# Kernel tuning notes

Measured on AMD Instinct MI355X. Metric: run time of the kernel, lower is better.

## Reference

```python
import jax, jax.numpy as jnp
import numpy as np

N, K, C, CL = 1024, 32, 64, 128
H = 2 * C  # MLP hidden = 2 * pair channels


def _ln(x, g, b, eps=1e-5):
    m = x.mean(-1, keepdims=True)
    v = jnp.mean(jnp.square(x - m), -1, keepdims=True)
    return (x - m) * jax.lax.rsqrt(v + eps) * g + b


def setup_inputs() -> dict:
    key = jax.random.key(0)
    ks = jax.random.split(key, 16)

    def w(k, shape):
        return jax.random.normal(k, shape, jnp.float32) / np.float32(np.sqrt(shape[0]))

    local = jax.random.normal(ks[0], (N, CL), jnp.float32)
    pair = jax.random.normal(ks[1], (N, N, C), jnp.float32)
    pair_update = jax.random.normal(ks[2], (N, K, C), jnp.float32)
    r = jax.random.randint(ks[3], (N, K), -(N // 4), N)
    neighbours = jnp.where(r < 0, -1, r)
    mask = jax.random.bernoulli(ks[4], 0.9, (N,))
    return dict(
        local=local, pair=pair, pair_update=pair_update,
        neighbours=neighbours, mask=mask,
        Wa=w(ks[5], (CL, C)), Wb=w(ks[6], (CL, C)),
        ln_g=jnp.ones((C,), jnp.float32), ln_b=jnp.zeros((C,), jnp.float32),
        W_aug=w(ks[7], (C, C)), W_lin=w(ks[8], (C, C)),
        W_left=w(ks[9], (C, 32)), b_left=jnp.zeros((32,), jnp.float32),
        W_right=w(ks[10], (C, 32)), b_right=jnp.zeros((32,), jnp.float32),
        W1=w(ks[11], (32, H)), W2=w(ks[12], (H, C)),
        W_int=w(ks[13], (CL, C)), b_int=jnp.zeros((C,), jnp.float32),
    )


def reference(local, pair, pair_update, neighbours, mask,
              Wa, Wb, ln_g, ln_b, W_aug, W_lin,
              W_left, b_left, W_right, b_right, W1, W2, W_int, b_int):
    idx = jnp.arange(pair.shape[0])
    # inject local info into the sparse pair update   [N,K,C]
    pu = pair_update + (local @ Wa)[:, None] + (local @ Wb)[neighbours]
    # gather neighbour pair features + layernorm      [N,K,C]
    lp = _ln(pair[idx[:, None], neighbours], ln_g, ln_b)
    lp = lp + pu @ W_aug
    linear = lp @ W_lin                               # [N,K,C]
    left = lp @ W_left + b_left                       # [N,K,32]
    right = lp @ W_right + b_right                    # [N,K,32]
    # neighbour-of-neighbour pair features            [N,K,K,32]
    npair = left[:, None] + right[neighbours]
    pn = neighbours[neighbours]                       # [N,K,K]
    pn = jnp.where((neighbours == -1)[:, :, None], pn, -1)
    pm = (pn != -1) & mask[pn] & (neighbours != -1)[:, None, :]
    # fused per-edge-pair MLP                          [N,K,K,C]
    upd = jax.nn.gelu(npair @ W1) @ W2
    # masked mean over the middle neighbour axis       [N,K,C]
    upd = jnp.where(pm[..., None], upd, 0.0).sum(axis=1)
    upd = upd / jnp.maximum(pm.sum(axis=1), 1).astype(upd.dtype)[..., None]
    inter = local @ W_int + b_int                     # [N,C]
    # scatter-add back into the dense pair tensor (collisions possible)
    return pair.at[idx[:, None], neighbours].add(upd + inter[:, None] + linear)
```

## Files before the change

### kernel.cpp

```cpp
#include <hip/hip_runtime.h>
#include <hip/hip_bf16.h>

constexpr int Nn  = 1024;
constexpr int Kk  = 32;
constexpr int Cc  = 64;
constexpr int CLl = 128;

__device__ __forceinline__ float gelu_tanh(float v){
  float c = 0.7978845608028654f*(v + 0.044715f*v*v*v);
  return 0.5f*v*(1.f + tanhf(c));
}

__global__ __launch_bounds__(64) void k0(
    const float* __restrict__ local, const float* __restrict__ Wa,
    const float* __restrict__ Wb, const float* __restrict__ Wint,
    const float* __restrict__ b_int,
    float* __restrict__ A, float* __restrict__ B, float* __restrict__ inter){
  int i = blockIdx.x;
  int c = threadIdx.x;
  __shared__ float l[CLl];
  l[c]      = local[i*CLl + c];
  l[c + 64] = local[i*CLl + 64 + c];
  __syncthreads();
  float a = 0.f, b = 0.f, t = 0.f;
  #pragma unroll 4
  for(int d = 0; d < CLl; ++d){
    float ld = l[d];
    a = fmaf(ld, Wa[d*Cc + c], a);
    b = fmaf(ld, Wb[d*Cc + c], b);
    t = fmaf(ld, Wint[d*Cc + c], t);
  }
  A[i*Cc + c] = a;
  B[i*Cc + c] = b;
  inter[i*Cc + c] = t + b_int[c];
}

__global__ __launch_bounds__(256) void k1(
    const float* __restrict__ pair, const float* __restrict__ pair_update,
    const int* __restrict__ neigh, const int* __restrict__ mask,
    const float* __restrict__ ln_g, const float* __restrict__ ln_b,
    const float* __restrict__ W_aug, const float* __restrict__ W_right,
    const float* __restrict__ b_right,
    const float* __restrict__ A, const float* __restrict__ B,
    float* __restrict__ r1023, int* __restrict__ qpart){
  const int i = Nn - 1;
  __shared__ float wA[4096];
  __shared__ float wR[2048];
  __shared__ float p [Kk][68];
  __shared__ float pu[Kk][68];
  __shared__ float lp[Kk][68];
  __shared__ int   nwS[Kk];
  __shared__ float ssum[Kk][9], ssq[Kk][9], stats[Kk][2];
  int tid = threadIdx.x;
  for(int idx = tid; idx < 4096; idx += 256) wA[idx] = W_aug[idx];
  for(int idx = tid; idx < 2048; idx += 256) wR[idx] = W_right[idx];
  if(tid < Kk){
    int n = neigh[i*Kk + tid];
    nwS[tid] = (n < 0) ? n + Nn : n;
    qpart[tid] = (n != -1 && mask[n] != 0) ? 1 : 0;
  }
  __syncthreads();
  int k = tid >> 3, s = tid & 7;
  {
    const float* prow = pair + ((size_t)i*Nn + nwS[k])*Cc + s*8;
    const float* pur  = pair_update + ((size_t)i*Kk + k)*Cc + s*8;
    const float* Ar = A + i*Cc + s*8;
    const float* Br = B + (size_t)nwS[k]*Cc + s*8;
    float ps = 0.f, ps2 = 0.f;
    for(int j = 0; j < 8; ++j){
      float v = prow[j];
      p[k][s*8 + j] = v; ps += v; ps2 += v*v;
      pu[k][s*8 + j] = pur[j] + Ar[j] + Br[j];
    }
    ssum[k][s] = ps; ssq[k][s] = ps2;
  }
  __syncthreads();
  if(s == 0){
    float m = 0.f, q = 0.f;
    for(int j = 0; j < 8; ++j){ m += ssum[k][j]; q += ssq[k][j]; }
    m *= (1.f/64.f); q *= (1.f/64.f);
    float var = fmaxf(q - m*m, 0.f);
    stats[k][0] = m; stats[k][1] = rsqrtf(var + 1e-5f);
  }
  __syncthreads();
  {
    float m = stats[k][0], r = stats[k][1];
    float acc[8];
    #pragma unroll
    for(int j = 0; j < 8; ++j){
      int c = s*8 + j;
      acc[j] = (p[k][c] - m)*r*ln_g[c] + ln_b[c];
    }
    for(int d = 0; d < 64; ++d){
      float pd = pu[k][d];
      #pragma unroll
      for(int j = 0; j < 8; ++j) acc[j] = fmaf(pd, wA[d*64 + s*8 + j], acc[j]);
    }
    #pragma unroll
    for(int j = 0; j < 8; ++j) lp[k][s*8 + j] = acc[j];
  }
  __syncthreads();
  {
    float acc[4] = {0.f,0.f,0.f,0.f};
    for(int d = 0; d < 64; ++d){
      float ld = lp[k][d];
      #pragma unroll
      for(int j = 0; j < 4; ++j) acc[j] = fmaf(ld, wR[d*32 + s*4 + j], acc[j]);
    }
    #pragma unroll
    for(int j = 0; j < 4; ++j)
      r1023[k*32 + s*4 + j] = acc[j] + b_right[s*4 + j];
  }
}

__global__ __launch_bounds__(256) void kcopy(
    const uint4* __restrict__ src, uint4* __restrict__ dst, int nvec){
  int idx = blockIdx.x*blockDim.x + threadIdx.x;
  int stride = gridDim.x*blockDim.x;
  for(; idx < nvec; idx += stride) dst[idx] = src[idx];
}

__global__ __launch_bounds__(256) void k2a(
    const float* __restrict__ pair, const float* __restrict__ pair_update,
    const int* __restrict__ neigh,
    const float* __restrict__ ln_g, const float* __restrict__ ln_b,
    const float* __restrict__ W_aug, const float* __restrict__ W_lin,
    const float* __restrict__ W_left, const float* __restrict__ b_left,
    const float* __restrict__ A, const float* __restrict__ B,
    const float* __restrict__ inter, const float* __restrict__ r1023,
    float* __restrict__ hG, float* __restrict__ linG){
  __shared__ float wA[4096];
  __shared__ float wL[4096];
  __shared__ float wF[2048];
  __shared__ float pbuf [Kk][68];
  __shared__ float pubuf[Kk][68];
  __shared__ float AiS[64], InS[64];
  __shared__ float ssum[Kk][9], ssq[Kk][9], stats[Kk][2];
  __shared__ int nwS[Kk];

  int i   = blockIdx.x;
  int tid = threadIdx.x;
  int k   = tid >> 3, s = tid & 7;

  for(int idx = tid; idx < 4096; idx += 256) wA[idx] = W_aug[idx];
  for(int idx = tid; idx < 4096; idx += 256) wL[idx] = W_lin[idx];
  for(int idx = tid; idx < 2048; idx += 256) wF[idx] = W_left[idx];
  if(tid < Kk){
    int n = neigh[i*Kk + tid];
    nwS[tid] = (n < 0) ? n + Nn : n;
  }
  if(tid < 64){ AiS[tid] = A[i*Cc + tid]; InS[tid] = inter[i*Cc + tid]; }
  __syncthreads();

  {
    const float4* p4 = (const float4*)(pair + ((size_t)i*Nn + nwS[k])*Cc) + s*2;
    float4 p0 = p4[0], p1 = p4[1];
    const float4* u4 = (const float4*)(pair_update + ((size_t)i*Kk + k)*Cc) + s*2;
    float4 u0 = u4[0], u1 = u4[1];
    const float4* Br = (const float4*)(B + (size_t)nwS[k]*Cc) + s*2;
    float4 b0 = Br[0], b1 = Br[1];
    float pf[8] = {p0.x,p0.y,p0.z,p0.w,p1.x,p1.y,p1.z,p1.w};
    float uf[8] = {u0.x,u0.y,u0.z,u0.w,u1.x,u1.y,u1.z,u1.w};
    float bv[8] = {b0.x,b0.y,b0.z,b0.w,b1.x,b1.y,b1.z,b1.w};
    float ps = 0.f, ps2 = 0.f;
    #pragma unroll
    for(int j = 0; j < 8; ++j){
      float v = pf[j];
      pbuf[k][s*8 + j] = v; ps += v; ps2 += v*v;
      pubuf[k][s*8 + j] = uf[j] + AiS[s*8 + j] + bv[j];
    }
    ssum[k][s] = ps; ssq[k][s] = ps2;
  }
  __syncthreads();

  if(s == 0){
    float m = 0.f, q = 0.f;
    for(int j = 0; j < 8; ++j){ m += ssum[k][j]; q += ssq[k][j]; }
    m *= (1.f/64.f); q *= (1.f/64.f);
    float var = fmaxf(q - m*m, 0.f);
    stats[k][0] = m; stats[k][1] = rsqrtf(var + 1e-5f);
  }
  __syncthreads();

  {
    float m = stats[k][0], r = stats[k][1];
    float acc[8];
    #pragma unroll
    for(int j = 0; j < 8; ++j){
      int c = s*8 + j;
      acc[j] = (pbuf[k][c] - m)*r*ln_g[c] + ln_b[c];
    }
    #pragma unroll 4
    for(int d = 0; d < 64; ++d){
      float pd = pubuf[k][d];
      #pragma unroll
      for(int j = 0; j < 8; ++j) acc[j] = fmaf(pd, wA[d*64 + s*8 + j], acc[j]);
    }
    #pragma unroll
    for(int j = 0; j < 8; ++j) pbuf[k][s*8 + j] = acc[j];
  }
  __syncthreads();

  {
    float accL[8] = {0,0,0,0,0,0,0,0};
    float accX[4] = {0,0,0,0};
    #pragma unroll 4
    for(int d = 0; d < 64; ++d){
      float ld = pbuf[k][d];
      #pragma unroll
      for(int j = 0; j < 8; ++j) accL[j] = fmaf(ld, wL[d*64 + s*8 + j], accL[j]);
      #pragma unroll
      for(int j = 0; j < 4; ++j) accX[j] = fmaf(ld, wF[d*32 + s*4 + j], accX[j]);
    }
    float4 rv = *(const float4*)(r1023 + k*32 + s*4);
    float rr[4] = {rv.x, rv.y, rv.z, rv.w};
    float* lo = linG + ((size_t)i*Kk + k)*Cc + s*8;
    #pragma unroll
    for(int j = 0; j < 8; ++j) lo[j] = accL[j] + InS[s*8 + j];
    float* ho = hG + ((size_t)i*Kk + k)*32 + s*4;
    #pragma unroll
    for(int j = 0; j < 4; ++j) ho[j] = accX[j] + b_left[s*4 + j] + rr[j];
  }
}

__global__ __launch_bounds__(256) void k2b(
    const float* __restrict__ pair, const int* __restrict__ neigh,
    const float* __restrict__ W1, const float* __restrict__ W2,
    const float* __restrict__ hG, const float* __restrict__ linG,
    const int* __restrict__ qpart,
    float* __restrict__ out){
  __shared__ float w1s[4096];
  __shared__ float w2s[8192];
  __shared__ float hbuf[Kk][36];
  __shared__ float cbuf[Kk][68];
  __shared__ int nbS[Kk], nwS[Kk], quS[Kk], leadS[Kk];
  __shared__ int cminus;

  int i   = blockIdx.x;
  int tid = threadIdx.x;
  int k   = tid >> 3, s = tid & 7;

  for(int idx = tid; idx < 4096; idx += 256) w1s[idx] = W1[idx];
  for(int idx = tid; idx < 8192; idx += 256) w2s[idx] = W2[idx];
  for(int idx = tid; idx < 1024; idx += 256)
    hbuf[idx >> 5][idx & 31] = hG[(size_t)i*1024 + idx];
  if(tid < Kk){
    int n = neigh[i*Kk + tid];
    nbS[tid] = n;
    nwS[tid] = (n < 0) ? n + Nn : n;
    quS[tid] = qpart[tid];
  }
  __syncthreads();
  if(tid == 0){
    int c = 0;
    for(int kk = 0; kk < Kk; ++kk) c |= (nbS[kk] == -1);
    cminus = c;
  }

  float gg[16];
  {
    float acc[16];
    #pragma unroll
    for(int j = 0; j < 16; ++j) acc[j] = 0.f;
    #pragma unroll 2
    for(int x = 0; x < 32; ++x){
      float hx = hbuf[k][x];
      #pragma unroll
      for(int j = 0; j < 16; ++j) acc[j] = fmaf(hx, w1s[x*128 + s*16 + j], acc[j]);
    }
    #pragma unroll
    for(int j = 0; j < 16; ++j) gg[j] = gelu_tanh(acc[j]);
  }
  __syncthreads();

  {
    float V[8] = {0,0,0,0,0,0,0,0};
    int klane = (k & 7) << 3;
    for(int ss = 0; ss < 8; ++ss){
      #pragma unroll
      for(int hh = 0; hh < 16; ++hh){
        float gv = __shfl(gg[hh], klane + ss, 64);
        int h = ss*16 + hh;
        #pragma unroll
        for(int j = 0; j < 8; ++j) V[j] = fmaf(gv, w2s[h*64 + s*8 + j], V[j]);
      }
    }
    const float4* l4 = (const float4*)(linG + ((size_t)i*Kk + k)*Cc) + s*2;
    float4 l0 = l4[0], l1 = l4[1];
    float lv[8] = {l0.x,l0.y,l0.z,l0.w,l1.x,l1.y,l1.z,l1.w};
    float mul = (cminus && quS[k] && nbS[k] != -1) ? 1.f : 0.f;
    #pragma unroll
    for(int j = 0; j < 8; ++j) cbuf[k][s*8 + j] = fmaf(mul, V[j], lv[j]);
  }
  __syncthreads();

  if(tid < Kk){
    int lead = 1;
    for(int kk = 0; kk < tid; ++kk) if(nwS[kk] == nwS[tid]) lead = 0;
    leadS[tid] = lead;
  }
  __syncthreads();
  if(leadS[k]){
    int col = nwS[k];
    float tot[8] = {0,0,0,0,0,0,0,0};
    for(int kk = 0; kk < Kk; ++kk){
      if(nwS[kk] == col){
        #pragma unroll
        for(int j = 0; j < 8; ++j) tot[j] += cbuf[kk][s*8 + j];
      }
    }
    size_t base = ((size_t)i*Nn + col)*Cc + s*8;
    const float4* pv = (const float4*)(pair + base);
    float4 p0 = pv[0], p1 = pv[1];
    float4 o0 = make_float4(p0.x+tot[0], p0.y+tot[1], p0.z+tot[2], p0.w+tot[3]);
    float4 o1 = make_float4(p1.x+tot[4], p1.y+tot[5], p1.z+tot[6], p1.w+tot[7]);
    float4* ov = (float4*)(out + base);
    ov[0] = o0; ov[1] = o1;
  }
}

extern "C" void kernel_launch(void* const* d_in, const int* in_sizes, int n_in,
                              void* d_out, int out_size, void* d_ws, size_t ws_size,
                              hipStream_t stream){
  (void)in_sizes; (void)n_in; (void)out_size; (void)ws_size;
  const float* local       = (const float*)d_in[0];
  const float* pair        = (const float*)d_in[1];
  const float* pair_update = (const float*)d_in[2];
  const int*   neighbours  = (const int*)d_in[3];
  const int*   mask        = (const int*)d_in[4];
  const float* Wa          = (const float*)d_in[5];
  const float* Wb          = (const float*)d_in[6];
  const float* ln_g        = (const float*)d_in[7];
  const float* ln_b        = (const float*)d_in[8];
  const float* W_aug       = (const float*)d_in[9];
  const float* W_lin       = (const float*)d_in[10];
  const float* W_left      = (const float*)d_in[11];
  const float* b_left      = (const float*)d_in[12];
  const float* W_right     = (const float*)d_in[13];
  const float* b_right     = (const float*)d_in[14];
  const float* W1          = (const float*)d_in[15];
  const float* W2          = (const float*)d_in[16];
  const float* W_int       = (const float*)d_in[17];
  const float* b_int       = (const float*)d_in[18];

  float* ws    = (float*)d_ws;
  float* A     = ws;
  float* B     = ws + 65536;
  float* inter = ws + 131072;
  float* r1023 = ws + 196608;
  int*   qpart = (int*)(ws + 197632);
  float* hG    = ws + 197664;
  float* linG  = ws + 1246240;

  k0<<<dim3(Nn), dim3(64), 0, stream>>>(local, Wa, Wb, W_int, b_int, A, B, inter);
  k1<<<dim3(1), dim3(256), 0, stream>>>(pair, pair_update, neighbours, mask,
                                        ln_g, ln_b, W_aug, W_right, b_right,
                                        A, B, r1023, qpart);
  k2a<<<dim3(Nn), dim3(256), 0, stream>>>(pair, pair_update, neighbours,
                                          ln_g, ln_b, W_aug, W_lin, W_left, b_left,
                                          A, B, inter, r1023, hG, linG);
  kcopy<<<dim3(8192), dim3(256), 0, stream>>>((const uint4*)pair, (uint4*)d_out,
                                              (Nn*Nn*Cc*4)/16);
  k2b<<<dim3(Nn), dim3(256), 0, stream>>>(pair, neighbours, W1, W2, hG, linG,
                                          qpart, (float*)d_out);
}
```

Baseline: 571.9 us.

## Fuse pair copy into update kernel and store weights as bf16 in LDS

Removes the separate full-tensor copy kernel: each block of the final kernel now copies its own row of the pair tensor to the output before scattering its updates, with a block barrier ordering the two writes. Weight matrices are converted to packed bf16 in shared memory, halving LDS footprint and load traffic. Threads are remapped so each one computes two neighbour rows, reusing every weight load across both. The bf16 weights lower accuracy of all the small matmuls, and the per-block copy is serialised with compute inside each block rather than run as a separate grid.

```diff
diff --git a/kernel.cpp b/kernel.cpp
--- a/kernel.cpp
+++ b/kernel.cpp
@@ -6,9 +6,20 @@
 constexpr int Cc  = 64;
 constexpr int CLl = 128;
 
+typedef unsigned int   u32;
+typedef unsigned short u16;
+
 __device__ __forceinline__ float gelu_tanh(float v){
   float c = 0.7978845608028654f*(v + 0.044715f*v*v*v);
   return 0.5f*v*(1.f + tanhf(c));
+}
+__device__ __forceinline__ float bflo(u32 u){ return __uint_as_float(u<<16); }
+__device__ __forceinline__ float bfhi(u32 u){ return __uint_as_float(u & 0xffff0000u); }
+__device__ __forceinline__ u32 pack_bf(float a, float b){
+  u32 xa = __float_as_uint(a), xb = __float_as_uint(b);
+  u32 ra = (xa + 0x7fffu + ((xa>>16)&1u)) >> 16;
+  u32 rb = (xb + 0x7fffu + ((xb>>16)&1u)) >> 16;
+  return ra | (rb<<16);
 }
 
 __global__ __launch_bounds__(64) void k0(
@@ -113,13 +124,6 @@
   }
 }
 
-__global__ __launch_bounds__(256) void kcopy(
-    const uint4* __restrict__ src, uint4* __restrict__ dst, int nvec){
-  int idx = blockIdx.x*blockDim.x + threadIdx.x;
-  int stride = gridDim.x*blockDim.x;
-  for(; idx < nvec; idx += stride) dst[idx] = src[idx];
-}
-
 __global__ __launch_bounds__(256) void k2a(
     const float* __restrict__ pair, const float* __restrict__ pair_update,
     const int* __restrict__ neigh,
@@ -129,35 +133,47 @@
     const float* __restrict__ A, const float* __restrict__ B,
     const float* __restrict__ inter, const float* __restrict__ r1023,
     float* __restrict__ hG, float* __restrict__ linG){
-  __shared__ float wA[4096];
-  __shared__ float wL[4096];
-  __shared__ float wF[2048];
+  __shared__ u32 wbA[2048];
+  __shared__ u32 wbL[2048];
+  __shared__ u32 wbF[1024];
   __shared__ float pbuf [Kk][68];
   __shared__ float pubuf[Kk][68];
-  __shared__ float AiS[64], InS[64];
+  __shared__ float AiS[64], InS[64], lgS[64], lbS[64];
   __shared__ float ssum[Kk][9], ssq[Kk][9], stats[Kk][2];
   __shared__ int nwS[Kk];
 
   int i   = blockIdx.x;
   int tid = threadIdx.x;
-  int k   = tid >> 3, s = tid & 7;
-
-  for(int idx = tid; idx < 4096; idx += 256) wA[idx] = W_aug[idx];
-  for(int idx = tid; idx < 4096; idx += 256) wL[idx] = W_lin[idx];
-  for(int idx = tid; idx < 2048; idx += 256) wF[idx] = W_left[idx];
+
+  for(int idx = tid; idx < 2048; idx += 256){
+    const float2 wa = *(const float2*)(W_aug + idx*2);
+    wbA[idx] = pack_bf(wa.x, wa.y);
+    const float2 wl = *(const float2*)(W_lin + idx*2);
+    wbL[idx] = pack_bf(wl.x, wl.y);
+  }
+  for(int idx = tid; idx < 1024; idx += 256){
+    const float2 wf = *(const float2*)(W_left + idx*2);
+    wbF[idx] = pack_bf(wf.x, wf.y);
+  }
   if(tid < Kk){
     int n = neigh[i*Kk + tid];
     nwS[tid] = (n < 0) ? n + Nn : n;
   }
-  if(tid < 64){ AiS[tid] = A[i*Cc + tid]; InS[tid] = inter[i*Cc + tid]; }
-  __syncthreads();
-
-  {
-    const float4* p4 = (const float4*)(pair + ((size_t)i*Nn + nwS[k])*Cc) + s*2;
+  if(tid < 64){
+    AiS[tid] = A[i*Cc + tid];
+    InS[tid] = inter[i*Cc + tid];
+    lgS[tid] = ln_g[tid];
+    lbS[tid] = ln_b[tid];
+  }
+  __syncthreads();
+
+  {
+    int k8 = tid >> 3, s8 = tid & 7;
+    const float4* p4 = (const float4*)(pair + ((size_t)i*Nn + nwS[k8])*Cc) + s8*2;
     float4 p0 = p4[0], p1 = p4[1];
-    const float4* u4 = (const float4*)(pair_update + ((size_t)i*Kk + k)*Cc) + s*2;
+    const float4* u4 = (const float4*)(pair_update + ((size_t)i*Kk + k8)*Cc) + s8*2;
     float4 u0 = u4[0], u1 = u4[1];
-    const float4* Br = (const float4*)(B + (size_t)nwS[k]*Cc) + s*2;
+    const float4* Br = (const float4*)(B + (size_t)nwS[k8]*Cc) + s8*2;
     float4 b0 = Br[0], b1 = Br[1];
     float pf[8] = {p0.x,p0.y,p0.z,p0.w,p1.x,p1.y,p1.z,p1.w};
     float uf[8] = {u0.x,u0.y,u0.z,u0.w,u1.x,u1.y,u1.z,u1.w};
@@ -166,71 +182,96 @@
     #pragma unroll
     for(int j = 0; j < 8; ++j){
       float v = pf[j];
-      pbuf[k][s*8 + j] = v; ps += v; ps2 += v*v;
-      pubuf[k][s*8 + j] = uf[j] + AiS[s*8 + j] + bv[j];
-    }
-    ssum[k][s] = ps; ssq[k][s] = ps2;
-  }
-  __syncthreads();
-
-  if(s == 0){
+      pbuf[k8][s8*8 + j] = v; ps += v; ps2 += v*v;
+      pubuf[k8][s8*8 + j] = uf[j] + AiS[s8*8 + j] + bv[j];
+    }
+    ssum[k8][s8] = ps; ssq[k8][s8] = ps2;
+  }
+  __syncthreads();
+
+  if((tid & 7) == 0){
+    int k8 = tid >> 3;
     float m = 0.f, q = 0.f;
-    for(int j = 0; j < 8; ++j){ m += ssum[k][j]; q += ssq[k][j]; }
+    for(int j = 0; j < 8; ++j){ m += ssum[k8][j]; q += ssq[k8][j]; }
     m *= (1.f/64.f); q *= (1.f/64.f);
     float var = fmaxf(q - m*m, 0.f);
-    stats[k][0] = m; stats[k][1] = rsqrtf(var + 1e-5f);
-  }
-  __syncthreads();
-
-  {
-    float m = stats[k][0], r = stats[k][1];
-    float acc[8];
-    #pragma unroll
-    for(int j = 0; j < 8; ++j){
-      int c = s*8 + j;
-      acc[j] = (pbuf[k][c] - m)*r*ln_g[c] + ln_b[c];
+    stats[k8][0] = m; stats[k8][1] = rsqrtf(var + 1e-5f);
+  }
+  __syncthreads();
+
+  int kq = tid >> 4;
+  int s  = tid & 15;
+  int k0 = kq, k1i = kq + 16;
+  int c0 = s*4;
+
+  float a0[4], a1[4];
+  {
+    float m0 = stats[k0][0], r0 = stats[k0][1];
+    float m1 = stats[k1i][0], r1 = stats[k1i][1];
+    #pragma unroll
+    for(int j = 0; j < 4; ++j){
+      int c = c0 + j;
+      a0[j] = (pbuf[k0][c]  - m0)*r0*lgS[c] + lbS[c];
+      a1[j] = (pbuf[k1i][c] - m1)*r1*lgS[c] + lbS[c];
     }
     #pragma unroll 4
     for(int d = 0; d < 64; ++d){
-      float pd = pubuf[k][d];
-      #pragma unroll
-      for(int j = 0; j < 8; ++j) acc[j] = fmaf(pd, wA[d*64 + s*8 + j], acc[j]);
-    }
-    #pragma unroll
-    for(int j = 0; j < 8; ++j) pbuf[k][s*8 + j] = acc[j];
-  }
-  __syncthreads();
-
-  {
-    float accL[8] = {0,0,0,0,0,0,0,0};
-    float accX[4] = {0,0,0,0};
+      uint2 wv = *(const uint2*)&wbA[d*32 + s*2];
+      float w0 = bflo(wv.x), w1 = bfhi(wv.x), w2 = bflo(wv.y), w3 = bfhi(wv.y);
+      float p0 = pubuf[k0][d], p1 = pubuf[k1i][d];
+      a0[0] = fmaf(p0, w0, a0[0]); a0[1] = fmaf(p0, w1, a0[1]);
+      a0[2] = fmaf(p0, w2, a0[2]); a0[3] = fmaf(p0, w3, a0[3]);
+      a1[0] = fmaf(p1, w0, a1[0]); a1[1] = fmaf(p1, w1, a1[1]);
+      a1[2] = fmaf(p1, w2, a1[2]); a1[3] = fmaf(p1, w3, a1[3]);
+    }
+  }
+  __syncthreads();
+  {
+    #pragma unroll
+    for(int j = 0; j < 4; ++j){ pbuf[k0][c0 + j] = a0[j]; pbuf[k1i][c0 + j] = a1[j]; }
+  }
+  __syncthreads();
+
+  {
+    float L0[4] = {0,0,0,0}, L1[4] = {0,0,0,0};
+    float X0[2] = {0,0},     X1[2] = {0,0};
     #pragma unroll 4
     for(int d = 0; d < 64; ++d){
-      float ld = pbuf[k][d];
-      #pragma unroll
-      for(int j = 0; j < 8; ++j) accL[j] = fmaf(ld, wL[d*64 + s*8 + j], accL[j]);
-      #pragma unroll
-      for(int j = 0; j < 4; ++j) accX[j] = fmaf(ld, wF[d*32 + s*4 + j], accX[j]);
-    }
-    float4 rv = *(const float4*)(r1023 + k*32 + s*4);
-    float rr[4] = {rv.x, rv.y, rv.z, rv.w};
-    float* lo = linG + ((size_t)i*Kk + k)*Cc + s*8;
-    #pragma unroll
-    for(int j = 0; j < 8; ++j) lo[j] = accL[j] + InS[s*8 + j];
-    float* ho = hG + ((size_t)i*Kk + k)*32 + s*4;
-    #pragma unroll
-    for(int j = 0; j < 4; ++j) ho[j] = accX[j] + b_left[s*4 + j] + rr[j];
-  }
-}
-
-__global__ __launch_bounds__(256) void k2b(
+      float p0 = pbuf[k0][d], p1 = pbuf[k1i][d];
+      uint2 wv = *(const uint2*)&wbL[d*32 + s*2];
+      float w0 = bflo(wv.x), w1 = bfhi(wv.x), w2 = bflo(wv.y), w3 = bfhi(wv.y);
+      L0[0] = fmaf(p0, w0, L0[0]); L0[1] = fmaf(p0, w1, L0[1]);
+      L0[2] = fmaf(p0, w2, L0[2]); L0[3] = fmaf(p0, w3, L0[3]);
+      L1[0] = fmaf(p1, w0, L1[0]); L1[1] = fmaf(p1, w1, L1[1]);
+      L1[2] = fmaf(p1, w2, L1[2]); L1[3] = fmaf(p1, w3, L1[3]);
+      u32 wf = wbF[d*16 + s];
+      float f0 = bflo(wf), f1 = bfhi(wf);
+      X0[0] = fmaf(p0, f0, X0[0]); X0[1] = fmaf(p0, f1, X0[1]);
+      X1[0] = fmaf(p1, f0, X1[0]); X1[1] = fmaf(p1, f1, X1[1]);
+    }
+    float4 o0 = make_float4(L0[0]+InS[c0], L0[1]+InS[c0+1], L0[2]+InS[c0+2], L0[3]+InS[c0+3]);
+    float4 o1 = make_float4(L1[0]+InS[c0], L1[1]+InS[c0+1], L1[2]+InS[c0+2], L1[3]+InS[c0+3]);
+    *(float4*)(linG + ((size_t)i*Kk + k0 )*Cc + c0) = o0;
+    *(float4*)(linG + ((size_t)i*Kk + k1i)*Cc + c0) = o1;
+    int x0 = s*2;
+    float2 bl = *(const float2*)(b_left + x0);
+    float2 rA = *(const float2*)(r1023 + k0*32  + x0);
+    float2 rB = *(const float2*)(r1023 + k1i*32 + x0);
+    float2 h0 = make_float2(X0[0] + bl.x + rA.x, X0[1] + bl.y + rA.y);
+    float2 h1 = make_float2(X1[0] + bl.x + rB.x, X1[1] + bl.y + rB.y);
+    *(float2*)(hG + ((size_t)i*Kk + k0 )*32 + x0) = h0;
+    *(float2*)(hG + ((size_t)i*Kk + k1i)*32 + x0) = h1;
+  }
+}
+
+__global__ __launch_bounds__(256) void kfuse(
     const float* __restrict__ pair, const int* __restrict__ neigh,
     const float* __restrict__ W1, const float* __restrict__ W2,
     const float* __restrict__ hG, const float* __restrict__ linG,
     const int* __restrict__ qpart,
     float* __restrict__ out){
-  __shared__ float w1s[4096];
-  __shared__ float w2s[8192];
+  __shared__ u32 w1b[2048];
+  __shared__ u32 w2b[4096];
   __shared__ float hbuf[Kk][36];
   __shared__ float cbuf[Kk][68];
   __shared__ int nbS[Kk], nwS[Kk], quS[Kk], leadS[Kk];
@@ -238,10 +279,22 @@
 
   int i   = blockIdx.x;
   int tid = threadIdx.x;
-  int k   = tid >> 3, s = tid & 7;
-
-  for(int idx = tid; idx < 4096; idx += 256) w1s[idx] = W1[idx];
-  for(int idx = tid; idx < 8192; idx += 256) w2s[idx] = W2[idx];
+
+  {
+    const float4* src = (const float4*)(pair + (size_t)i*Nn*Cc);
+    float4*       dst = (float4*)(out + (size_t)i*Nn*Cc);
+    #pragma unroll 4
+    for(int idx = tid; idx < 16384; idx += 256) dst[idx] = src[idx];
+  }
+
+  for(int idx = tid; idx < 2048; idx += 256){
+    const float2 w1 = *(const float2*)(W1 + idx*2);
+    w1b[idx] = pack_bf(w1.x, w1.y);
+    const float2 wa = *(const float2*)(W2 + idx*2);
+    w2b[idx] = pack_bf(wa.x, wa.y);
+    const float2 wb2 = *(const float2*)(W2 + 4096 + idx*2);
+    w2b[2048 + idx] = pack_bf(wb2.x, wb2.y);
+  }
   for(int idx = tid; idx < 1024; idx += 256)
     hbuf[idx >> 5][idx & 31] = hG[(size_t)i*1024 + idx];
   if(tid < Kk){
@@ -257,40 +310,62 @@
     cminus = c;
   }
 
-  float gg[16];
-  {
-    float acc[16];
-    #pragma unroll
-    for(int j = 0; j < 16; ++j) acc[j] = 0.f;
+  int kq = tid >> 4;
+  int s  = tid & 15;
+
+  float g0[8], g1v[8];
+  {
+    float A0[8], A1[8];
+    #pragma unroll
+    for(int j = 0; j < 8; ++j){ A0[j] = 0.f; A1[j] = 0.f; }
     #pragma unroll 2
     for(int x = 0; x < 32; ++x){
-      float hx = hbuf[k][x];
+      float h0 = hbuf[kq][x], h1 = hbuf[kq+16][x];
+      uint4 wv = *(const uint4*)&w1b[x*64 + s*4];
+      float w[8] = {bflo(wv.x),bfhi(wv.x),bflo(wv.y),bfhi(wv.y),
+                    bflo(wv.z),bfhi(wv.z),bflo(wv.w),bfhi(wv.w)};
       #pragma unroll
-      for(int j = 0; j < 16; ++j) acc[j] = fmaf(hx, w1s[x*128 + s*16 + j], acc[j]);
-    }
-    #pragma unroll
-    for(int j = 0; j < 16; ++j) gg[j] = gelu_tanh(acc[j]);
-  }
-  __syncthreads();
-
-  {
-    float V[8] = {0,0,0,0,0,0,0,0};
-    int klane = (k & 7) << 3;
-    for(int ss = 0; ss < 8; ++ss){
+      for(int j = 0; j < 8; ++j){
+        A0[j] = fmaf(h0, w[j], A0[j]);
+        A1[j] = fmaf(h1, w[j], A1[j]);
+      }
+    }
+    #pragma unroll
+    for(int j = 0; j < 8; ++j){ g0[j] = gelu_tanh(A0[j]); g1v[j] = gelu_tanh(A1[j]); }
+  }
+  __syncthreads();
+
+  {
+    float V0[4] = {0,0,0,0}, V1[4] = {0,0,0,0};
+    int lbase = (kq & 3) << 4;
+    for(int hb = 0; hb < 16; ++hb){
+      int src = lbase | hb;
       #pragma unroll
-      for(int hh = 0; hh < 16; ++hh){
-        float gv = __shfl(gg[hh], klane + ss, 64);
-        int h = ss*16 + hh;
-        #pragma unroll
-        for(int j = 0; j < 8; ++j) V[j] = fmaf(gv, w2s[h*64 + s*8 + j], V[j]);
+      for(int hj = 0; hj < 8; ++hj){
+        float gA = __shfl(g0[hj],  src, 64);
+        float gB = __shfl(g1v[hj], src, 64);
+        int h = hb*8 + hj;
+        uint2 wv = *(const uint2*)&w2b[h*32 + s*2];
+        float w0 = bflo(wv.x), w1 = bfhi(wv.x), w2 = bflo(wv.y), w3 = bfhi(wv.y);
+        V0[0] = fmaf(gA, w0, V0[0]); V0[1] = fmaf(gA, w1, V0[1]);
+        V0[2] = fmaf(gA, w2, V0[2]); V0[3] = fmaf(gA, w3, V0[3]);
+        V1[0] = fmaf(gB, w0, V1[0]); V1[1] = fmaf(gB, w1, V1[1]);
+        V1[2] = fmaf(gB, w2, V1[2]); V1[3] = fmaf(gB, w3, V1[3]);
       }
     }
-    const float4* l4 = (const float4*)(linG + ((size_t)i*Kk + k)*Cc) + s*2;
-    float4 l0 = l4[0], l1 = l4[1];
-    float lv[8] = {l0.x,l0.y,l0.z,l0.w,l1.x,l1.y,l1.z,l1.w};
-    float mul = (cminus && quS[k] && nbS[k] != -1) ? 1.f : 0.f;
-    #pragma unroll
-    for(int j = 0; j < 8; ++j) cbuf[k][s*8 + j] = fmaf(mul, V[j], lv[j]);
+    int c0 = s*4;
+    float4 l0 = *(const float4*)(linG + ((size_t)i*Kk + kq     )*Cc + c0);
+    float4 l1 = *(const float4*)(linG + ((size_t)i*Kk + kq + 16)*Cc + c0);
+    float mul0 = (cminus && quS[kq]      && nbS[kq]      != -1) ? 1.f : 0.f;
+    float mul1 = (cminus && quS[kq + 16] && nbS[kq + 16] != -1) ? 1.f : 0.f;
+    cbuf[kq][c0+0] = fmaf(mul0, V0[0], l0.x);
+    cbuf[kq][c0+1] = fmaf(mul0, V0[1], l0.y);
+    cbuf[kq][c0+2] = fmaf(mul0, V0[2], l0.z);
+    cbuf[kq][c0+3] = fmaf(mul0, V0[3], l0.w);
+    cbuf[kq+16][c0+0] = fmaf(mul1, V1[0], l1.x);
+    cbuf[kq+16][c0+1] = fmaf(mul1, V1[1], l1.y);
+    cbuf[kq+16][c0+2] = fmaf(mul1, V1[2], l1.z);
+    cbuf[kq+16][c0+3] = fmaf(mul1, V1[3], l1.w);
   }
   __syncthreads();
 
@@ -300,22 +375,25 @@
     leadS[tid] = lead;
   }
   __syncthreads();
-  if(leadS[k]){
-    int col = nwS[k];
-    float tot[8] = {0,0,0,0,0,0,0,0};
-    for(int kk = 0; kk < Kk; ++kk){
-      if(nwS[kk] == col){
-        #pragma unroll
-        for(int j = 0; j < 8; ++j) tot[j] += cbuf[kk][s*8 + j];
+  {
+    int k8 = tid >> 3, s8 = tid & 7;
+    if(leadS[k8]){
+      int col = nwS[k8];
+      float tot[8] = {0,0,0,0,0,0,0,0};
+      for(int kk = 0; kk < Kk; ++kk){
+        if(nwS[kk] == col){
+          #pragma unroll
+          for(int j = 0; j < 8; ++j) tot[j] += cbuf[kk][s8*8 + j];
+        }
       }
-    }
-    size_t base = ((size_t)i*Nn + col)*Cc + s*8;
-    const float4* pv = (const float4*)(pair + base);
-    float4 p0 = pv[0], p1 = pv[1];
-    float4 o0 = make_float4(p0.x+tot[0], p0.y+tot[1], p0.z+tot[2], p0.w+tot[3]);
-    float4 o1 = make_float4(p1.x+tot[4], p1.y+tot[5], p1.z+tot[6], p1.w+tot[7]);
-    float4* ov = (float4*)(out + base);
-    ov[0] = o0; ov[1] = o1;
+      size_t base = ((size_t)i*Nn + col)*Cc + s8*8;
+      const float4* pv = (const float4*)(pair + base);
+      float4 p0 = pv[0], p1 = pv[1];
+      float4 o0 = make_float4(p0.x+tot[0], p0.y+tot[1], p0.z+tot[2], p0.w+tot[3]);
+      float4 o1 = make_float4(p1.x+tot[4], p1.y+tot[5], p1.z+tot[6], p1.w+tot[7]);
+      float4* ov = (float4*)(out + base);
+      ov[0] = o0; ov[1] = o1;
+    }
   }
 }
 
@@ -359,8 +437,6 @@
   k2a<<<dim3(Nn), dim3(256), 0, stream>>>(pair, pair_update, neighbours,
                                           ln_g, ln_b, W_aug, W_lin, W_left, b_left,
                                           A, B, inter, r1023, hG, linG);
-  kcopy<<<dim3(8192), dim3(256), 0, stream>>>((const uint4*)pair, (uint4*)d_out,
-                                              (Nn*Nn*Cc*4)/16);
-  k2b<<<dim3(Nn), dim3(256), 0, stream>>>(pair, neighbours, W1, W2, hG, linG,
-                                          qpart, (float*)d_out);
-}
+  kfuse<<<dim3(Nn), dim3(256), 0, stream>>>(pair, neighbours, W1, W2, hG, linG,
+                                            qpart, (float*)d_out);
+}
```

Measured after the change: 546.8 us. -4.4%, faster.
